# Kernel tuning notes

Hardware: AMD Instinct MI355X
Metric: run time of the kernel (lower is better)

Reference implementation:

```python
import jax, jax.numpy as jnp
import numpy as np

N_NODES = 100000


def gcn_conv(x, edge_index, W, b):
    """PyG GCNConv: add self-loops, symmetric deg^-1/2 normalization, linear."""
    n = x.shape[0]
    h = x @ W  # [N, out]
    loop = jnp.arange(n, dtype=edge_index.dtype)
    src = jnp.concatenate([edge_index[0], loop])
    dst = jnp.concatenate([edge_index[1], loop])
    deg = jax.ops.segment_sum(jnp.ones_like(dst, dtype=h.dtype), dst, num_segments=n)
    dinv = jnp.where(deg > 0, jax.lax.rsqrt(deg), 0.0)
    norm = dinv[src] * dinv[dst]  # [E+N]
    msg = h[src] * norm[:, None]  # gather + scale
    out = jax.ops.segment_sum(msg, dst, num_segments=n)  # scatter-add
    return out + b


def setup_inputs() -> dict:
    key = jax.random.key(0)
    k1, k2, k3, k4 = jax.random.split(key, 4)
    d_in, d_hid, d_out = 128, 128, 128  # output_dim // 2 = 128
    E = 1600000
    x = jax.random.normal(k1, (N_NODES, d_in), dtype=jnp.float32)
    edge_index = jax.random.randint(k2, (2, E), 0, N_NODES, dtype=jnp.int64)
    s1 = 1.0 / np.sqrt(d_in)
    s2 = 1.0 / np.sqrt(d_hid)
    W1 = jax.random.normal(k3, (d_in, d_hid), dtype=jnp.float32) * s1
    b1 = jnp.zeros((d_hid,), dtype=jnp.float32)
    W2 = jax.random.normal(k4, (d_hid, d_out), dtype=jnp.float32) * s2
    b2 = jnp.zeros((d_out,), dtype=jnp.float32)
    return {"x": x, "edge_index": edge_index, "W1": W1, "b1": b1, "W2": W2, "b2": b2}


def reference(x, edge_index, W1, b1, W2, b2):
    h = jax.nn.relu(gcn_conv(x, edge_index, W1, b1))
    # dropout(p=0.5) is identity in eval mode
    return gcn_conv(h, edge_index, W2, b2)
```

## Files before the change

### kernel.cpp

```cpp
#include <hip/hip_runtime.h>

#define D 128

typedef unsigned int uint;
typedef unsigned short ushort;
typedef __attribute__((ext_vector_type(8))) short bf16x8_t;
typedef __attribute__((ext_vector_type(4))) float f32x4_t;

#define BSH 9
#define BMASK 511
#define BN 512
#define CAP 9216
#define CHUNK 2048
#define NBUCKP 256

__device__ inline uint bf16rn(float f) {
    uint u = __float_as_uint(f);
    return (u + 0x7fffu + ((u >> 16) & 1u)) >> 16;
}

__global__ __launch_bounds__(256) void kp_scatter3(const int* __restrict__ src,
                                                   const int* __restrict__ dst,
                                                   int* __restrict__ gcnt,
                                                   uint* __restrict__ bkt, int E, int nbuck) {
    __shared__ uint stage[CHUNK];
    __shared__ int cnt[NBUCKP], loc[NBUCKP], cnt2[NBUCKP], gbase[NBUCKP];
    int t = threadIdx.x;
    int base = blockIdx.x * CHUNK;
    int end = min(E, base + CHUNK);

    cnt[t] = 0; cnt2[t] = 0; gbase[t] = 0;
    __syncthreads();
    for (int i = base + t; i < end; i += 256)
        atomicAdd(&cnt[dst[i] >> BSH], 1);
    __syncthreads();
    int v = cnt[t];
    loc[t] = v;
    __syncthreads();
    for (int off = 1; off < NBUCKP; off <<= 1) {
        int x = (t >= off) ? loc[t - off] : 0;
        __syncthreads();
        loc[t] += x;
        __syncthreads();
    }
    if (t < nbuck && cnt[t] > 0)
        gbase[t] = atomicAdd(&gcnt[t], cnt[t]);
    __syncthreads();
    for (int i = base + t; i < end; i += 256) {
        int d = dst[i], s = src[i];
        int bk = d >> BSH;
        int r = atomicAdd(&cnt2[bk], 1);
        stage[(loc[bk] - cnt[bk]) + r] = ((uint)s << BSH) | (uint)(d & BMASK);
    }
    __syncthreads();
    int grp = t >> 4, gl = t & 15;
    for (int bk = grp; bk < nbuck; bk += 16) {
        int c = cnt[bk];
        if (c == 0) continue;
        int lo = loc[bk] - c;
        int gb = gbase[bk];
        uint* ob = bkt + (size_t)bk * CAP;
        for (int j = gl; j < c; j += 16) {
            int di = gb + j;
            if (di < CAP) ob[di] = stage[lo + j];
        }
    }
}

__global__ __launch_bounds__(512) void kp_build3(uint* __restrict__ bkt,
                                                 const int* __restrict__ gcnt,
                                                 int2* __restrict__ row_se,
                                                 float* __restrict__ dinv, int n, int nbuck,
                                                 const float* __restrict__ W1,
                                                 const float* __restrict__ W2,
                                                 ushort* __restrict__ W1h, ushort* __restrict__ W1l,
                                                 ushort* __restrict__ W2h, ushort* __restrict__ W2l) {
    int t = threadIdx.x, b = blockIdx.x;
    if (b >= nbuck) {
        int i = (b - nbuck) * 512 + t;
        int sel = i >> 14;
        int j = i & 16383;
        int k = j >> 7, nn = j & 127;
        const float* W = sel ? W2 : W1;
        float w = W[k * D + nn];
        uint hb = bf16rn(w);
        float hf = __uint_as_float(hb << 16);
        uint lb = bf16rn(w - hf);
        if (sel) { W2h[nn * D + k] = (ushort)hb; W2l[nn * D + k] = (ushort)lb; }
        else     { W1h[nn * D + k] = (ushort)hb; W1l[nn * D + k] = (ushort)lb; }
        return;
    }
    __shared__ uint ents[CAP];
    __shared__ int cnt[BN], loc[BN], cnt2[BN];
    int m = gcnt[b];
    if (m > CAP) m = CAP;
    uint* bk = bkt + (size_t)b * CAP;
    for (int i = t; i < m; i += 512) ents[i] = bk[i];
    cnt[t] = 0; cnt2[t] = 0;
    __syncthreads();
    for (int i = t; i < m; i += 512) atomicAdd(&cnt[ents[i] & BMASK], 1);
    __syncthreads();
    int v = cnt[t];
    loc[t] = v;
    __syncthreads();
    for (int off = 1; off < BN; off <<= 1) {
        int x = (t >= off) ? loc[t - off] : 0;
        __syncthreads();
        loc[t] += x;
        __syncthreads();
    }
    int base = b * CAP;
    int node = (b << BSH) + t;
    if (node < n) {
        row_se[node] = make_int2(base + loc[t] - v, base + loc[t]);
        dinv[node] = rsqrtf((float)(v + 1));
    }
    __syncthreads();
    for (int i = t; i < m; i += 512) {
        uint p = ents[i];
        int low = p & BMASK;
        int r = atomicAdd(&cnt2[low], 1);
        ((int*)bk)[(loc[low] - cnt[low]) + r] = (int)((p >> BSH) << 8);
    }
}

__device__ inline void accum_bf16x8(float* a, uint4 v) {
    a[0] += __uint_as_float(v.x << 16);
    a[1] += __uint_as_float(v.x & 0xffff0000u);
    a[2] += __uint_as_float(v.y << 16);
    a[3] += __uint_as_float(v.y & 0xffff0000u);
    a[4] += __uint_as_float(v.z << 16);
    a[5] += __uint_as_float(v.z & 0xffff0000u);
    a[6] += __uint_as_float(v.w << 16);
    a[7] += __uint_as_float(v.w & 0xffff0000u);
}

template <bool A_FP32>
__global__ __launch_bounds__(256, 2) void k_gemm_mfma(const void* __restrict__ A,
                                                      const ushort* __restrict__ Wth,
                                                      const ushort* __restrict__ Wtl,
                                                      const float* __restrict__ dinv,
                                                      ushort* __restrict__ Yb, int M) {
    constexpr int STR = 72;
    constexpr int TILE = 128 * STR;
    __shared__ ushort lds[A_FP32 ? 4 * TILE : 3 * TILE];
    ushort* Ah = lds;
    ushort* Wh = lds + TILE;
    ushort* Wl = lds + 2 * TILE;
    ushort* Al = A_FP32 ? (lds + 3 * TILE) : nullptr;

    int t = threadIdx.x;
    int lane = t & 63, wave = t >> 6;
    int quad = lane >> 4, l16 = lane & 15;
    int m_off = (wave & 1) * 64;
    int n_off = (wave >> 1) * 64;
    int block_row = blockIdx.x * 128;

    f32x4_t acc[4][4];
#pragma unroll
    for (int mt = 0; mt < 4; mt++)
#pragma unroll
        for (int nt = 0; nt < 4; nt++) acc[mt][nt] = (f32x4_t){0.f, 0.f, 0.f, 0.f};

    for (int kc = 0; kc < 128; kc += 64) {
        if (A_FP32) {
            const float* Af = (const float*)A;
#pragma unroll
            for (int it = 0; it < 8; it++) {
                int s = t + it * 256;
                int row = s >> 4, kl = (s & 15) * 4;
                int gr = block_row + row;
                float4 v = make_float4(0.f, 0.f, 0.f, 0.f);
                if (gr < M) v = *(const float4*)(Af + (size_t)gr * D + kc + kl);
                ushort4 h, l;
                uint hb, lb; float hf;
                hb = bf16rn(v.x); hf = __uint_as_float(hb << 16); lb = bf16rn(v.x - hf);
                h.x = (ushort)hb; l.x = (ushort)lb;
                hb = bf16rn(v.y); hf = __uint_as_float(hb << 16); lb = bf16rn(v.y - hf);
                h.y = (ushort)hb; l.y = (ushort)lb;
                hb = bf16rn(v.z); hf = __uint_as_float(hb << 16); lb = bf16rn(v.z - hf);
                h.z = (ushort)hb; l.z = (ushort)lb;
                hb = bf16rn(v.w); hf = __uint_as_float(hb << 16); lb = bf16rn(v.w - hf);
                h.w = (ushort)hb; l.w = (ushort)lb;
                *(ushort4*)&Ah[row * STR + kl] = h;
                *(ushort4*)&Al[row * STR + kl] = l;
            }
        } else {
            const ushort* Ab = (const ushort*)A;
#pragma unroll
            for (int it = 0; it < 4; it++) {
                int s = t + it * 256;
                int row = s >> 3, kl = (s & 7) * 8;
                int gr = block_row + row;
                uint4 v = make_uint4(0u, 0u, 0u, 0u);
                if (gr < M) v = *(const uint4*)(Ab + (size_t)gr * D + kc + kl);
                *(uint4*)&Ah[row * STR + kl] = v;
            }
        }
#pragma unroll
        for (int it = 0; it < 4; it++) {
            int s = t + it * 256;
            int nrow = s >> 3, kl = (s & 7) * 8;
            *(uint4*)&Wh[nrow * STR + kl] = *(const uint4*)(Wth + nrow * D + kc + kl);
            *(uint4*)&Wl[nrow * STR + kl] = *(const uint4*)(Wtl + nrow * D + kc + kl);
        }
        __syncthreads();

#pragma unroll
        for (int ks = 0; ks < 2; ks++) {
            int kf = ks * 32 + quad * 8;
            bf16x8_t ah[4], bh[4], bl[4];
#pragma unroll
            for (int mt = 0; mt < 4; mt++)
                ah[mt] = *(const bf16x8_t*)&Ah[(m_off + mt * 16 + l16) * STR + kf];
#pragma unroll
            for (int nt = 0; nt < 4; nt++) {
                bh[nt] = *(const bf16x8_t*)&Wh[(n_off + nt * 16 + l16) * STR + kf];
                bl[nt] = *(const bf16x8_t*)&Wl[(n_off + nt * 16 + l16) * STR + kf];
            }
            if (A_FP32) {
                bf16x8_t al[4];
#pragma unroll
                for (int mt = 0; mt < 4; mt++)
                    al[mt] = *(const bf16x8_t*)&Al[(m_off + mt * 16 + l16) * STR + kf];
#pragma unroll
                for (int mt = 0; mt < 4; mt++)
#pragma unroll
                    for (int nt = 0; nt < 4; nt++) {
                        acc[mt][nt] = __builtin_amdgcn_mfma_f32_16x16x32_bf16(ah[mt], bh[nt], acc[mt][nt], 0, 0, 0);
                        acc[mt][nt] = __builtin_amdgcn_mfma_f32_16x16x32_bf16(al[mt], bh[nt], acc[mt][nt], 0, 0, 0);
                        acc[mt][nt] = __builtin_amdgcn_mfma_f32_16x16x32_bf16(ah[mt], bl[nt], acc[mt][nt], 0, 0, 0);
                    }
            } else {
#pragma unroll
                for (int mt = 0; mt < 4; mt++)
#pragma unroll
                    for (int nt = 0; nt < 4; nt++) {
                        acc[mt][nt] = __builtin_amdgcn_mfma_f32_16x16x32_bf16(ah[mt], bh[nt], acc[mt][nt], 0, 0, 0);
                        acc[mt][nt] = __builtin_amdgcn_mfma_f32_16x16x32_bf16(ah[mt], bl[nt], acc[mt][nt], 0, 0, 0);
                    }
            }
        }
        __syncthreads();
    }

#pragma unroll
    for (int mt = 0; mt < 4; mt++) {
#pragma unroll
        for (int reg = 0; reg < 4; reg++) {
            int gr = block_row + m_off + mt * 16 + quad * 4 + reg;
            if (gr < M) {
                float di = dinv[gr];
#pragma unroll
                for (int nt = 0; nt < 4; nt++) {
                    int colg = n_off + nt * 16 + l16;
                    Yb[(size_t)gr * D + colg] = (ushort)bf16rn(di * acc[mt][nt][reg]);
                }
            }
        }
    }
}

__global__ __launch_bounds__(256) void k_agg(const ushort* __restrict__ Hb,
                                             const int2* __restrict__ row_se,
                                             const int* __restrict__ colb,
                                             const float* __restrict__ dinv,
                                             const float* __restrict__ bias,
                                             float* __restrict__ Yf, ushort* __restrict__ Yb,
                                             int n, int do_relu, int out_bf16) {
    __shared__ int ls[4][64];
    int wv = threadIdx.x >> 6;
    int node = blockIdx.x * 4 + wv;
    int lane = threadIdx.x & 63;
    int chain = lane >> 4;
    int l16   = lane & 15;
    if (node >= n) return;

    int2 se = row_se[node];
    int start = se.x, end = se.y;

    float a0[8], a1[8];
#pragma unroll
    for (int k = 0; k < 8; k++) { a0[k] = 0.f; a1[k] = 0.f; }

    const char* hbase = (const char*)Hb;
    uint loff = (uint)l16 * 16u;

    if (chain == 0) {
        uint4 v = *(const uint4*)(hbase + (uint)node * 256u + loff);
        accum_bf16x8(a0, v);
    }

    for (int tb = start; tb < end; tb += 64) {
        int idx = tb + lane;
        ls[wv][lane] = (idx < end) ? colb[idx] : 0;
        int c = min(64, end - tb);
        int j = chain;
        for (; j + 12 < c; j += 16) {
            uint o0 = (uint)ls[wv][j];
            uint o1 = (uint)ls[wv][j + 4];
            uint o2 = (uint)ls[wv][j + 8];
            uint o3 = (uint)ls[wv][j + 12];
            uint4 v0 = *(const uint4*)(hbase + o0 + loff);
            uint4 v1 = *(const uint4*)(hbase + o1 + loff);
            uint4 v2 = *(const uint4*)(hbase + o2 + loff);
            uint4 v3 = *(const uint4*)(hbase + o3 + loff);
            accum_bf16x8(a0, v0);
            accum_bf16x8(a1, v1);
            accum_bf16x8(a0, v2);
            accum_bf16x8(a1, v3);
        }
        for (; j + 4 < c; j += 8) {
            uint o0 = (uint)ls[wv][j];
            uint o1 = (uint)ls[wv][j + 4];
            uint4 v0 = *(const uint4*)(hbase + o0 + loff);
            uint4 v1 = *(const uint4*)(hbase + o1 + loff);
            accum_bf16x8(a0, v0);
            accum_bf16x8(a1, v1);
        }
        if (j < c) {
            uint o0 = (uint)ls[wv][j];
            uint4 v0 = *(const uint4*)(hbase + o0 + loff);
            accum_bf16x8(a0, v0);
        }
    }

    float acc[8];
#pragma unroll
    for (int k = 0; k < 8; k++) {
        float v = a0[k] + a1[k];
        v += __shfl_xor(v, 16, 64);
        v += __shfl_xor(v, 32, 64);
        acc[k] = v;
    }

    if (chain == 0) {
        float di = dinv[node];
        const float4* bp = (const float4*)bias + l16 * 2;
        float4 b0 = bp[0], b1 = bp[1];
        float o[8];
        o[0] = fmaf(di, acc[0], b0.x); o[1] = fmaf(di, acc[1], b0.y);
        o[2] = fmaf(di, acc[2], b0.z); o[3] = fmaf(di, acc[3], b0.w);
        o[4] = fmaf(di, acc[4], b1.x); o[5] = fmaf(di, acc[5], b1.y);
        o[6] = fmaf(di, acc[6], b1.z); o[7] = fmaf(di, acc[7], b1.w);
        if (do_relu) {
#pragma unroll
            for (int k = 0; k < 8; k++) o[k] = fmaxf(o[k], 0.f);
        }
        if (out_bf16) {
            uint4 pk;
            pk.x = bf16rn(o[0]) | (bf16rn(o[1]) << 16);
            pk.y = bf16rn(o[2]) | (bf16rn(o[3]) << 16);
            pk.z = bf16rn(o[4]) | (bf16rn(o[5]) << 16);
            pk.w = bf16rn(o[6]) | (bf16rn(o[7]) << 16);
            ((uint4*)(Yb + (size_t)node * D))[l16] = pk;
        } else {
            f32x4_t q0 = {o[0], o[1], o[2], o[3]};
            f32x4_t q1 = {o[4], o[5], o[6], o[7]};
            f32x4_t* yp = (f32x4_t*)(Yf + (size_t)node * D) + l16 * 2;
            __builtin_nontemporal_store(q0, yp);
            __builtin_nontemporal_store(q1, yp + 1);
        }
    }
}

extern "C" void kernel_launch(void* const* d_in, const int* in_sizes, int n_in,
                              void* d_out, int out_size, void* d_ws, size_t ws_size,
                              hipStream_t stream) {
    const float* x  = (const float*)d_in[0];
    const int*   ei = (const int*)d_in[1];
    const float* W1 = (const float*)d_in[2];
    const float* b1 = (const float*)d_in[3];
    const float* W2 = (const float*)d_in[4];
    const float* b2 = (const float*)d_in[5];
    float* out = (float*)d_out;

    int n = in_sizes[0] / D;
    int E = in_sizes[1] / 2;
    const int* src = ei;
    const int* dst = ei + E;

    int nbuck = (n + BMASK) >> BSH;

    char* p = (char*)d_ws;
    ushort* h_buf = (ushort*)p; p += (size_t)n * D * sizeof(ushort);
    ushort* y_buf = (ushort*)p; p += (size_t)n * D * sizeof(ushort);
    ushort* w1h   = (ushort*)p; p += (size_t)D * D * sizeof(ushort);
    ushort* w1l   = (ushort*)p; p += (size_t)D * D * sizeof(ushort);
    ushort* w2h   = (ushort*)p; p += (size_t)D * D * sizeof(ushort);
    ushort* w2l   = (ushort*)p; p += (size_t)D * D * sizeof(ushort);
    uint*  bkt    = (uint*)p;   p += (size_t)nbuck * CAP * sizeof(uint);
    float* dinv   = (float*)p;  p += (size_t)n * sizeof(float);
    int2*  row_se = (int2*)p;   p += (size_t)n * sizeof(int2);
    int*   gcnt   = (int*)p;    p += (size_t)nbuck * sizeof(int);

    (void)hipMemsetAsync(gcnt, 0, (size_t)nbuck * sizeof(int), stream);
    int sc_grid = (E + CHUNK - 1) / CHUNK;
    kp_scatter3<<<sc_grid, 256, 0, stream>>>(src, dst, gcnt, bkt, E, nbuck);
    kp_build3<<<nbuck + 64, 512, 0, stream>>>(bkt, gcnt, row_se, dinv, n, nbuck,
                                              W1, W2, w1h, w1l, w2h, w2l);

    int gemm_grid = (n + 127) / 128;
    int agg_grid  = (n + 3) / 4;
    const int* colp = (const int*)bkt;

    k_gemm_mfma<true><<<gemm_grid, 256, 0, stream>>>(x, w1h, w1l, dinv, h_buf, n);
    k_agg<<<agg_grid, 256, 0, stream>>>(h_buf, row_se, colp, dinv, b1, nullptr, y_buf, n, 1, 1);
    k_gemm_mfma<false><<<gemm_grid, 256, 0, stream>>>(y_buf, w2h, w2l, dinv, h_buf, n);
    k_agg<<<agg_grid, 256, 0, stream>>>(h_buf, row_se, colp, dinv, b2, out, nullptr, n, 0, 0);
}
```

Baseline: 325.5 us.

## Reuse atomic ranks in bucketing kernels and widen GEMM blocks to 512 threads

The scatter kernel now loads each edge once into registers and keeps the rank returned by the first shared-memory atomic, which removes the second dst/src read pass and the second atomic pass. The build kernel likewise stores per-entry ranks in LDS so the second atomic counter is no longer needed. Separately, the MFMA GEMM moves from 256 to 512 threads per block, with each wave covering a 64x32 output tile instead of 64x64, to raise wave count and occupancy. This costs extra LDS for the ranks array and gives less register-level reuse of the A fragments per wave in the GEMM.

```diff
diff --git a/kernel.cpp b/kernel.cpp
--- a/kernel.cpp
+++ b/kernel.cpp
@@ -24,15 +24,26 @@
                                                    int* __restrict__ gcnt,
                                                    uint* __restrict__ bkt, int E, int nbuck) {
     __shared__ uint stage[CHUNK];
-    __shared__ int cnt[NBUCKP], loc[NBUCKP], cnt2[NBUCKP], gbase[NBUCKP];
+    __shared__ int cnt[NBUCKP], loc[NBUCKP], gbase[NBUCKP];
     int t = threadIdx.x;
     int base = blockIdx.x * CHUNK;
     int end = min(E, base + CHUNK);
 
-    cnt[t] = 0; cnt2[t] = 0; gbase[t] = 0;
-    __syncthreads();
-    for (int i = base + t; i < end; i += 256)
-        atomicAdd(&cnt[dst[i] >> BSH], 1);
+    cnt[t] = 0; gbase[t] = 0;
+    __syncthreads();
+    uint pk[8]; int bk[8]; int rk[8];
+#pragma unroll
+    for (int it = 0; it < 8; it++) {
+        int i = base + t + it * 256;
+        if (i < end) {
+            int d = dst[i], s = src[i];
+            bk[it] = d >> BSH;
+            pk[it] = ((uint)s << BSH) | (uint)(d & BMASK);
+            rk[it] = atomicAdd(&cnt[bk[it]], 1);
+        } else {
+            bk[it] = 0; pk[it] = 0u; rk[it] = -1;
+        }
+    }
     __syncthreads();
     int v = cnt[t];
     loc[t] = v;
@@ -46,20 +57,18 @@
     if (t < nbuck && cnt[t] > 0)
         gbase[t] = atomicAdd(&gcnt[t], cnt[t]);
     __syncthreads();
-    for (int i = base + t; i < end; i += 256) {
-        int d = dst[i], s = src[i];
-        int bk = d >> BSH;
-        int r = atomicAdd(&cnt2[bk], 1);
-        stage[(loc[bk] - cnt[bk]) + r] = ((uint)s << BSH) | (uint)(d & BMASK);
-    }
+#pragma unroll
+    for (int it = 0; it < 8; it++)
+        if (rk[it] >= 0)
+            stage[(loc[bk[it]] - cnt[bk[it]]) + rk[it]] = pk[it];
     __syncthreads();
     int grp = t >> 4, gl = t & 15;
-    for (int bk = grp; bk < nbuck; bk += 16) {
-        int c = cnt[bk];
+    for (int b2 = grp; b2 < nbuck; b2 += 16) {
+        int c = cnt[b2];
         if (c == 0) continue;
-        int lo = loc[bk] - c;
-        int gb = gbase[bk];
-        uint* ob = bkt + (size_t)bk * CAP;
+        int lo = loc[b2] - c;
+        int gb = gbase[b2];
+        uint* ob = bkt + (size_t)b2 * CAP;
         for (int j = gl; j < c; j += 16) {
             int di = gb + j;
             if (di < CAP) ob[di] = stage[lo + j];
@@ -91,14 +100,18 @@
         return;
     }
     __shared__ uint ents[CAP];
-    __shared__ int cnt[BN], loc[BN], cnt2[BN];
+    __shared__ ushort ranks[CAP];
+    __shared__ int cnt[BN], loc[BN];
     int m = gcnt[b];
     if (m > CAP) m = CAP;
     uint* bk = bkt + (size_t)b * CAP;
     for (int i = t; i < m; i += 512) ents[i] = bk[i];
-    cnt[t] = 0; cnt2[t] = 0;
-    __syncthreads();
-    for (int i = t; i < m; i += 512) atomicAdd(&cnt[ents[i] & BMASK], 1);
+    cnt[t] = 0;
+    __syncthreads();
+    for (int i = t; i < m; i += 512) {
+        int r = atomicAdd(&cnt[ents[i] & BMASK], 1);
+        ranks[i] = (ushort)r;
+    }
     __syncthreads();
     int v = cnt[t];
     loc[t] = v;
@@ -119,8 +132,7 @@
     for (int i = t; i < m; i += 512) {
         uint p = ents[i];
         int low = p & BMASK;
-        int r = atomicAdd(&cnt2[low], 1);
-        ((int*)bk)[(loc[low] - cnt[low]) + r] = (int)((p >> BSH) << 8);
+        ((int*)bk)[(loc[low] - cnt[low]) + (int)ranks[i]] = (int)((p >> BSH) << 8);
     }
 }
 
@@ -136,7 +148,7 @@
 }
 
 template <bool A_FP32>
-__global__ __launch_bounds__(256, 2) void k_gemm_mfma(const void* __restrict__ A,
+__global__ __launch_bounds__(512, 4) void k_gemm_mfma(const void* __restrict__ A,
                                                       const ushort* __restrict__ Wth,
                                                       const ushort* __restrict__ Wtl,
                                                       const float* __restrict__ dinv,
@@ -152,22 +164,22 @@
     int t = threadIdx.x;
     int lane = t & 63, wave = t >> 6;
     int quad = lane >> 4, l16 = lane & 15;
-    int m_off = (wave & 1) * 64;
-    int n_off = (wave >> 1) * 64;
+    int m_off = (wave >> 2) * 64;
+    int n_off = (wave & 3) * 32;
     int block_row = blockIdx.x * 128;
 
-    f32x4_t acc[4][4];
+    f32x4_t acc[4][2];
 #pragma unroll
     for (int mt = 0; mt < 4; mt++)
 #pragma unroll
-        for (int nt = 0; nt < 4; nt++) acc[mt][nt] = (f32x4_t){0.f, 0.f, 0.f, 0.f};
+        for (int nt = 0; nt < 2; nt++) acc[mt][nt] = (f32x4_t){0.f, 0.f, 0.f, 0.f};
 
     for (int kc = 0; kc < 128; kc += 64) {
         if (A_FP32) {
             const float* Af = (const float*)A;
 #pragma unroll
-            for (int it = 0; it < 8; it++) {
-                int s = t + it * 256;
+            for (int it = 0; it < 4; it++) {
+                int s = t + it * 512;
                 int row = s >> 4, kl = (s & 15) * 4;
                 int gr = block_row + row;
                 float4 v = make_float4(0.f, 0.f, 0.f, 0.f);
@@ -188,8 +200,8 @@
         } else {
             const ushort* Ab = (const ushort*)A;
 #pragma unroll
-            for (int it = 0; it < 4; it++) {
-                int s = t + it * 256;
+            for (int it = 0; it < 2; it++) {
+                int s = t + it * 512;
                 int row = s >> 3, kl = (s & 7) * 8;
                 int gr = block_row + row;
                 uint4 v = make_uint4(0u, 0u, 0u, 0u);
@@ -198,8 +210,8 @@
             }
         }
 #pragma unroll
-        for (int it = 0; it < 4; it++) {
-            int s = t + it * 256;
+        for (int it = 0; it < 2; it++) {
+            int s = t + it * 512;
             int nrow = s >> 3, kl = (s & 7) * 8;
             *(uint4*)&Wh[nrow * STR + kl] = *(const uint4*)(Wth + nrow * D + kc + kl);
             *(uint4*)&Wl[nrow * STR + kl] = *(const uint4*)(Wtl + nrow * D + kc + kl);
@@ -209,12 +221,12 @@
 #pragma unroll
         for (int ks = 0; ks < 2; ks++) {
             int kf = ks * 32 + quad * 8;
-            bf16x8_t ah[4], bh[4], bl[4];
+            bf16x8_t ah[4], bh[2], bl[2];
 #pragma unroll
             for (int mt = 0; mt < 4; mt++)
                 ah[mt] = *(const bf16x8_t*)&Ah[(m_off + mt * 16 + l16) * STR + kf];
 #pragma unroll
-            for (int nt = 0; nt < 4; nt++) {
+            for (int nt = 0; nt < 2; nt++) {
                 bh[nt] = *(const bf16x8_t*)&Wh[(n_off + nt * 16 + l16) * STR + kf];
                 bl[nt] = *(const bf16x8_t*)&Wl[(n_off + nt * 16 + l16) * STR + kf];
             }
@@ -226,7 +238,7 @@
 #pragma unroll
                 for (int mt = 0; mt < 4; mt++)
 #pragma unroll
-                    for (int nt = 0; nt < 4; nt++) {
+                    for (int nt = 0; nt < 2; nt++) {
                         acc[mt][nt] = __builtin_amdgcn_mfma_f32_16x16x32_bf16(ah[mt], bh[nt], acc[mt][nt], 0, 0, 0);
                         acc[mt][nt] = __builtin_amdgcn_mfma_f32_16x16x32_bf16(al[mt], bh[nt], acc[mt][nt], 0, 0, 0);
                         acc[mt][nt] = __builtin_amdgcn_mfma_f32_16x16x32_bf16(ah[mt], bl[nt], acc[mt][nt], 0, 0, 0);
@@ -235,7 +247,7 @@
 #pragma unroll
                 for (int mt = 0; mt < 4; mt++)
 #pragma unroll
-                    for (int nt = 0; nt < 4; nt++) {
+                    for (int nt = 0; nt < 2; nt++) {
                         acc[mt][nt] = __builtin_amdgcn_mfma_f32_16x16x32_bf16(ah[mt], bh[nt], acc[mt][nt], 0, 0, 0);
                         acc[mt][nt] = __builtin_amdgcn_mfma_f32_16x16x32_bf16(ah[mt], bl[nt], acc[mt][nt], 0, 0, 0);
                     }
@@ -252,7 +264,7 @@
             if (gr < M) {
                 float di = dinv[gr];
 #pragma unroll
-                for (int nt = 0; nt < 4; nt++) {
+                for (int nt = 0; nt < 2; nt++) {
                     int colg = n_off + nt * 16 + l16;
                     Yb[(size_t)gr * D + colg] = (ushort)bf16rn(di * acc[mt][nt][reg]);
                 }
@@ -404,8 +416,8 @@
     int agg_grid  = (n + 3) / 4;
     const int* colp = (const int*)bkt;
 
-    k_gemm_mfma<true><<<gemm_grid, 256, 0, stream>>>(x, w1h, w1l, dinv, h_buf, n);
+    k_gemm_mfma<true><<<gemm_grid, 512, 0, stream>>>(x, w1h, w1l, dinv, h_buf, n);
     k_agg<<<agg_grid, 256, 0, stream>>>(h_buf, row_se, colp, dinv, b1, nullptr, y_buf, n, 1, 1);
-    k_gemm_mfma<false><<<gemm_grid, 256, 0, stream>>>(y_buf, w2h, w2l, dinv, h_buf, n);
+    k_gemm_mfma<false><<<gemm_grid, 512, 0, stream>>>(y_buf, w2h, w2l, dinv, h_buf, n);
     k_agg<<<agg_grid, 256, 0, stream>>>(h_buf, row_se, colp, dinv, b2, out, nullptr, n, 0, 0);
 }
```

Result: faster. 312.2 us (-4.1%).
